# Kernel tuning notes

Measured on AMD Instinct MI355X. Metric: run time of the kernel, lower is better.

Reference implementation:

```python
import jax, jax.numpy as jnp
import numpy as np

B, T, V, E, H, O = 32, 512, 32000, 512, 1024, 128


def setup_inputs() -> dict:
    key = jax.random.key(0)
    ks = jax.random.split(key, 8)
    s = lambda k, shape: (jax.random.normal(k, shape) * 0.02).astype(jnp.float32)
    return {
        "tokens": jax.random.randint(ks[0], (B, T), 0, V),
        "verb_indices": jax.random.randint(ks[1], (B,), 0, T),
        "emb": s(ks[2], (V, E)),
        "W_ih": s(ks[3], (4 * H, E)),
        "W_hh": s(ks[4], (4 * H, H)),
        "b_ih": jnp.zeros((4 * H,), jnp.float32),
        "b_hh": jnp.zeros((4 * H,), jnp.float32),
        "W_lin": s(ks[5], (O, 2 * H)),
        "b_lin": jnp.zeros((O,), jnp.float32),
    }


def _lstm(e, W_ih, W_hh, b_ih, b_hh):
    # e: [B,T,E] -> hidden states [B,T,H]; PyTorch gate order i,f,g,o
    Hd = W_hh.shape[1]
    # precompute input projections for all timesteps (one big GEMM)
    x_proj = jnp.einsum("bte,ge->btg", e, W_ih) + b_ih + b_hh  # [B,T,4H]

    def step(carry, x_t):
        h, c = carry
        gates = x_t + h @ W_hh.T  # [B,4H]
        i, f, g, o = jnp.split(gates, 4, axis=-1)
        i = jax.nn.sigmoid(i)
        f = jax.nn.sigmoid(f)
        g = jnp.tanh(g)
        o = jax.nn.sigmoid(o)
        c = f * c + i * g
        h = o * jnp.tanh(c)
        return (h, c), h

    h0 = jnp.zeros((e.shape[0], Hd), e.dtype)
    (_, _), hs = jax.lax.scan(step, (h0, h0), jnp.swapaxes(x_proj, 0, 1))
    return jnp.swapaxes(hs, 0, 1)  # [B,T,H]


def reference(tokens, verb_indices, emb, W_ih, W_hh, b_ih, b_hh, W_lin, b_lin):
    e = emb[tokens]  # [B,T,E]
    out = _lstm(e, W_ih, W_hh, b_ih, b_hh)  # [B,T,H]
    verbs = out[jnp.arange(out.shape[0]), verb_indices]  # [B,H] verb hidden state
    # linear over concat([verb, out_t]) == split the weight and sum two GEMMs
    Wv, Wo = jnp.split(W_lin, 2, axis=1)  # [O,H] each
    logits = (
        jnp.einsum("bh,oh->bo", verbs, Wv)[:, None, :]
        + jnp.einsum("bth,oh->bto", out, Wo)
        + b_lin
    )  # [B,T,O]
    return jax.nn.log_softmax(logits, axis=-1)
```

## Files before the change

### kernel.cpp

```cpp
#include <hip/hip_runtime.h>


typedef short s8v __attribute__((ext_vector_type(8)));
typedef float f4v __attribute__((ext_vector_type(4)));
typedef unsigned int u4v __attribute__((ext_vector_type(4)));

#define WS_CNT_OFF   131072
#define WS_VROWS_OFF 139264
#define WS_VLOG_OFF  204800

__device__ __forceinline__ float b2f(unsigned short u) {
    union { unsigned int i; float f; } x; x.i = ((unsigned int)u) << 16; return x.f;
}
__device__ __forceinline__ unsigned short f2b(float f) {
    union { float f; unsigned int i; } x; x.f = f;
    unsigned int r = (x.i + 0x7fffu + ((x.i >> 16) & 1u)) >> 16;
    return (unsigned short)r;
}
__device__ __forceinline__ float blo(unsigned int u) {
    union { unsigned int i; float f; } x; x.i = u << 16; return x.f;
}
__device__ __forceinline__ float bhi(unsigned int u) {
    union { unsigned int i; float f; } x; x.i = u & 0xffff0000u; return x.f;
}

__global__ void init_kernel(unsigned int* ws) {
    int i = blockIdx.x * 256 + threadIdx.x;
    if (i < 34816) ws[i] = 0u;
}

__device__ __forceinline__ void project_cols(
    const short* hA, const float* __restrict__ Wr0, const float* __restrict__ Wr1,
    float* __restrict__ dout, int b0, int tproj, int w, int tid)
{
    const int pair = tid >> 4, p = tid & 15;
    const int b = pair >> 1, oc = pair & 1;
    const float* wr = oc ? Wr1 : Wr0;
    float acc = 0.f;
#pragma unroll
    for (int j = 0; j < 8; ++j) {
        int ko = j * 16 + p;
        u4v d = *(const u4v*)&hA[(ko * 17 + b) * 8];
        const float* wk = wr + ko * 8;
        f4v w0 = *(const f4v*)wk, w1 = *(const f4v*)(wk + 4);
        unsigned int d0 = d[0], d1 = d[1], d2 = d[2], d3 = d[3];
        acc += blo(d0) * w0[0] + bhi(d0) * w0[1] + blo(d1) * w0[2] + bhi(d1) * w0[3]
             + blo(d2) * w1[0] + bhi(d2) * w1[1] + blo(d3) * w1[2] + bhi(d3) * w1[3];
    }
#pragma unroll
    for (int off = 1; off < 16; off <<= 1) acc += __shfl_xor(acc, off);
    if (p == 0)
        dout[((size_t)(b0 + b) * 512 + tproj) * 128 + 2 * w + oc] = acc;
}

__global__ __launch_bounds__(256, 1) void scan_kernel(
    const int* __restrict__ tokens,
    const int* __restrict__ vidx,
    const float* __restrict__ emb,
    const float* __restrict__ W_ih,
    const float* __restrict__ W_hh,
    const float* __restrict__ b_ih,
    const float* __restrict__ b_hh,
    const float* __restrict__ W_lin,
    unsigned short* __restrict__ hbuf,
    unsigned int* __restrict__ flags_all,
    unsigned short* __restrict__ vrows,
    float* __restrict__ dout)
{
    __shared__ short hA[128 * 17 * 8];
    __shared__ short eA[2][64 * 17 * 8];
    __shared__ int   tokL[512 * 8];

    const int tid  = threadIdx.x;
    const int g    = blockIdx.x >> 6;
    const int w    = blockIdx.x & 63;
    const int b0   = g * 8;
    const int lane = tid & 63;
    const int v    = tid >> 6;
    const int q    = lane >> 4;
    const int c    = lane & 15;

    const float* Wr0 = W_lin + (size_t)(2 * w) * 2048 + 1024;
    const float* Wr1 = W_lin + (size_t)(2 * w + 1) * 2048 + 1024;

    const int n = ((c >> 2) * 1024) + 16 * w + 4 * v + (c & 3);
    s8v Bh[32], Be[16];
    {
        const float* rh = W_hh + (size_t)n * 1024;
#pragma unroll
        for (int ks = 0; ks < 32; ++ks) {
            const float* s = rh + ks * 32 + q * 8;
            f4v lo = *(const f4v*)s, hi = *(const f4v*)(s + 4);
            s8v f;
#pragma unroll
            for (int j = 0; j < 4; ++j) { f[j] = (short)f2b(lo[j]); f[j + 4] = (short)f2b(hi[j]); }
            Bh[ks] = f;
        }
        const float* re = W_ih + (size_t)n * 512;
#pragma unroll
        for (int ks = 0; ks < 16; ++ks) {
            const float* s = re + ks * 32 + q * 8;
            f4v lo = *(const f4v*)s, hi = *(const f4v*)(s + 4);
            s8v f;
#pragma unroll
            for (int j = 0; j < 4; ++j) { f[j] = (short)f2b(lo[j]); f[j + 4] = (short)f2b(hi[j]); }
            Be[ks] = f;
        }
    }

    for (int i = tid; i < 4096; i += 256)
        tokL[(i & 511) * 8 + (i >> 9)] = tokens[(b0 + (i >> 9)) * 512 + (i & 511)];

    const s8v zv = {0,0,0,0,0,0,0,0};
    for (int i = tid; i < 1024; i += 256) { int ko = i >> 3, r = 8 + (i & 7);
        *(s8v*)&hA[(ko * 17 + r) * 8] = zv; }
    for (int i = tid; i < 512; i += 256) { int ko = i >> 3, r = 8 + (i & 7);
        *(s8v*)&eA[0][(ko * 17 + r) * 8] = zv;
        *(s8v*)&eA[1][(ko * 17 + r) * 8] = zv; }
    __syncthreads();

    for (int i = tid; i < 512; i += 256) {
        int ko = i >> 3, b = i & 7;
        int tok = tokL[b];
        const float* s = emb + (size_t)tok * 512 + ko * 8;
        f4v lo = *(const f4v*)s, hi = *(const f4v*)(s + 4);
        s8v f;
#pragma unroll
        for (int j = 0; j < 4; ++j) { f[j] = (short)f2b(lo[j]); f[j + 4] = (short)f2b(hi[j]); }
        *(s8v*)&eA[0][(ko * 17 + b) * 8] = f;
    }

    const int jloc = 16 * w + 4 * v + (lane & 3);
    const float bI = b_ih[jloc]        + b_hh[jloc];
    const float bF = b_ih[1024 + jloc] + b_hh[1024 + jloc];
    const float bG = b_ih[2048 + jloc] + b_hh[2048 + jloc];
    const float bO = b_ih[3072 + jloc] + b_hh[3072 + jloc];
    const int  shbase = (lane & 48) | (lane & 3);
    const bool stAct  = ((lane & 12) == 0) && (lane < 32) && !(lane & 1);
    const int  phid   = 8 * w + 2 * v + ((lane >> 1) & 1);
    const int  Db     = (phid >> 2) * 32 + (phid & 3) + (lane >> 4) * 16;
    int tv0 = -1, tv1 = -1, tv2 = -1, tv3 = -1;
    if (stAct) {
        int bb = b0 + 4 * (lane >> 4);
        tv0 = vidx[bb]; tv1 = vidx[bb + 1]; tv2 = vidx[bb + 2]; tv3 = vidx[bb + 3];
    }
    const int vrb = (b0 + 4 * (lane >> 4)) * 1024 + jloc;

    float cst[4] = {0.f, 0.f, 0.f, 0.f};
    unsigned short* hb     = hbuf + g * 2 * 8192;
    unsigned int*   hb32   = (unsigned int*)hb;
    unsigned int*   gflags = flags_all + g * 256;
    int rp = 0;
    __syncthreads();

    for (int t = 0; t < 512; ++t) {
        f4v ae = {0.f, 0.f, 0.f, 0.f};
        const short* eAc = eA[t & 1];
#pragma unroll
        for (int ks = 0; ks < 16; ++ks) {
            s8v a = *(const s8v*)&eAc[((ks * 4 + q) * 17 + c) * 8];
            ae = __builtin_amdgcn_mfma_f32_16x16x32_bf16(a, Be[ks], ae, 0, 0, 0);
        }

        if (t > 0) {
            const unsigned tt = (unsigned)t;
            for (;;) {
                unsigned f0 = __hip_atomic_load(&gflags[lane],       __ATOMIC_RELAXED, __HIP_MEMORY_SCOPE_AGENT);
                unsigned f1 = __hip_atomic_load(&gflags[64 + lane],  __ATOMIC_RELAXED, __HIP_MEMORY_SCOPE_AGENT);
                unsigned f2 = __hip_atomic_load(&gflags[128 + lane], __ATOMIC_RELAXED, __HIP_MEMORY_SCOPE_AGENT);
                unsigned f3 = __hip_atomic_load(&gflags[192 + lane], __ATOMIC_RELAXED, __HIP_MEMORY_SCOPE_AGENT);
                unsigned m01 = f0 < f1 ? f0 : f1;
                unsigned m23 = f2 < f3 ? f2 : f3;
                unsigned m = m01 < m23 ? m01 : m23;
                if (__all(m >= tt)) break;
            }
            asm volatile("" ::: "memory");
        }

        {
            const unsigned long long* src =
                (const unsigned long long*)(hb + rp * 8192);
#pragma unroll
            for (int it = 0; it < 8; ++it) {
                int j = it * 256 + tid;
                unsigned long long d = __hip_atomic_load(src + j, __ATOMIC_RELAXED,
                                                         __HIP_MEMORY_SCOPE_AGENT);
                int ko = j >> 4, b = (j >> 1) & 7, posq = (j & 1) << 2;
                *(unsigned long long*)&hA[(ko * 17 + b) * 8 + posq] = d;
            }
        }
        __syncthreads();

        f4v ah0 = {0.f, 0.f, 0.f, 0.f}, ah1 = {0.f, 0.f, 0.f, 0.f};
#pragma unroll
        for (int ks = 0; ks < 16; ++ks) {
            s8v a0 = *(const s8v*)&hA[((2 * ks) * 4 + q) * 17 * 8 + c * 8];
            s8v a1 = *(const s8v*)&hA[((2 * ks + 1) * 4 + q) * 17 * 8 + c * 8];
            ah0 = __builtin_amdgcn_mfma_f32_16x16x32_bf16(a0, Bh[2 * ks], ah0, 0, 0, 0);
            ah1 = __builtin_amdgcn_mfma_f32_16x16x32_bf16(a1, Bh[2 * ks + 1], ah1, 0, 0, 0);
        }

        int hui[4];
#pragma unroll
        for (int r = 0; r < 4; ++r) {
            float s = ae[r] + ah0[r] + ah1[r];
            float xi = __shfl(s, shbase);
            float xf = __shfl(s, shbase + 4);
            float xg = __shfl(s, shbase + 8);
            float xo = __shfl(s, shbase + 12);
            float ig = 1.f / (1.f + __expf(-(xi + bI)));
            float fg = 1.f / (1.f + __expf(-(xf + bF)));
            float gg = 1.f - 2.f / (1.f + __expf(2.f * (xg + bG)));
            float og = 1.f / (1.f + __expf(-(xo + bO)));
            cst[r] = fg * cst[r] + ig * gg;
            float h = og * (1.f - 2.f / (1.f + __expf(2.f * cst[r])));
            hui[r] = (int)f2b(h);
        }
#pragma unroll
        for (int r = 0; r < 4; ++r) {
            int ph = __shfl_xor(hui[r], 1);
            if (stAct) {
                unsigned pack = (unsigned)hui[r] | (((unsigned)ph) << 16);
                __hip_atomic_store(&hb32[(rp ^ 1) * 4096 + Db + r * 4], pack,
                                   __ATOMIC_RELAXED, __HIP_MEMORY_SCOPE_AGENT);
                int tvr = (r == 0) ? tv0 : (r == 1) ? tv1 : (r == 2) ? tv2 : tv3;
                if (t == tvr)
                    *(unsigned int*)&vrows[vrb + r * 1024] = pack;
            }
        }
        asm volatile("s_waitcnt vmcnt(0)" ::: "memory");
        if (lane == 0)
            __hip_atomic_store(&gflags[w * 4 + v], (unsigned)(t + 1),
                               __ATOMIC_RELAXED, __HIP_MEMORY_SCOPE_AGENT);

        if (t >= 1)
            project_cols(hA, Wr0, Wr1, dout, b0, t - 1, w, tid);

        if (t < 511) {
            int tn = t + 1;
            short* eAn = eA[tn & 1];
            for (int i = tid; i < 512; i += 256) {
                int ko = i >> 3, b = i & 7;
                int tok = tokL[tn * 8 + b];
                const float* s2 = emb + (size_t)tok * 512 + ko * 8;
                f4v lo = *(const f4v*)s2, hi = *(const f4v*)(s2 + 4);
                s8v f;
#pragma unroll
                for (int j2 = 0; j2 < 4; ++j2) { f[j2] = (short)f2b(lo[j2]); f[j2 + 4] = (short)f2b(hi[j2]); }
                *(s8v*)&eAn[(ko * 17 + b) * 8] = f;
            }
        }
        __syncthreads();
        rp ^= 1;
    }

    for (;;) {
        unsigned f0 = __hip_atomic_load(&gflags[lane],       __ATOMIC_RELAXED, __HIP_MEMORY_SCOPE_AGENT);
        unsigned f1 = __hip_atomic_load(&gflags[64 + lane],  __ATOMIC_RELAXED, __HIP_MEMORY_SCOPE_AGENT);
        unsigned f2 = __hip_atomic_load(&gflags[128 + lane], __ATOMIC_RELAXED, __HIP_MEMORY_SCOPE_AGENT);
        unsigned f3 = __hip_atomic_load(&gflags[192 + lane], __ATOMIC_RELAXED, __HIP_MEMORY_SCOPE_AGENT);
        unsigned m01 = f0 < f1 ? f0 : f1;
        unsigned m23 = f2 < f3 ? f2 : f3;
        unsigned m = m01 < m23 ? m01 : m23;
        if (__all(m >= 512u)) break;
    }
    asm volatile("" ::: "memory");
    {
        const unsigned long long* src = (const unsigned long long*)(hb + rp * 8192);
#pragma unroll
        for (int it = 0; it < 8; ++it) {
            int j = it * 256 + tid;
            unsigned long long d = __hip_atomic_load(src + j, __ATOMIC_RELAXED,
                                                     __HIP_MEMORY_SCOPE_AGENT);
            int ko = j >> 4, b = (j >> 1) & 7, posq = (j & 1) << 2;
            *(unsigned long long*)&hA[(ko * 17 + b) * 8 + posq] = d;
        }
    }
    __syncthreads();
    project_cols(hA, Wr0, Wr1, dout, b0, 511, w, tid);
}

__global__ void verb_kernel(const unsigned short* __restrict__ vrows,
                            const float* __restrict__ W_lin,
                            const float* __restrict__ b_lin,
                            float* __restrict__ vlog)
{
    __shared__ float vrow[1024];
    int b = blockIdx.x, tid = threadIdx.x;
    for (int i = tid; i < 1024; i += 256) vrow[i] = b2f(vrows[b * 1024 + i]);
    __syncthreads();
    if (tid < 128) {
        float acc = 0.f;
        const float* wr = W_lin + (size_t)tid * 2048;
        for (int h = 0; h < 1024; ++h) acc += vrow[h] * wr[h];
        vlog[b * 128 + tid] = acc + b_lin[tid];
    }
}

__global__ void softmax_kernel(float* __restrict__ dout,
                               const float* __restrict__ vlog)
{
    int tid = threadIdx.x;
    int grow = blockIdx.x * 32 + (tid >> 3);
    int part = tid & 7;
    int b = grow >> 9;
    float* pp = dout + (size_t)grow * 128 + part * 16;
    const float* vb = vlog + b * 128 + part * 16;
    float L[16];
#pragma unroll
    for (int i = 0; i < 16; ++i) L[i] = pp[i] + vb[i];
    float m = L[0];
#pragma unroll
    for (int i = 1; i < 16; ++i) m = fmaxf(m, L[i]);
    for (int off = 1; off < 8; off <<= 1) m = fmaxf(m, __shfl_xor(m, off));
    float s = 0.f;
#pragma unroll
    for (int i = 0; i < 16; ++i) s += expf(L[i] - m);
    for (int off = 1; off < 8; off <<= 1) s += __shfl_xor(s, off);
    float lz = m + logf(s);
#pragma unroll
    for (int i = 0; i < 16; ++i) pp[i] = L[i] - lz;
}

extern "C" void kernel_launch(void* const* d_in, const int* in_sizes, int n_in,
                              void* d_out, int out_size, void* d_ws, size_t ws_size,
                              hipStream_t stream) {
    const int*   tokens = (const int*)d_in[0];
    const int*   vidx   = (const int*)d_in[1];
    const float* emb    = (const float*)d_in[2];
    const float* W_ih   = (const float*)d_in[3];
    const float* W_hh   = (const float*)d_in[4];
    const float* b_ih   = (const float*)d_in[5];
    const float* b_hh   = (const float*)d_in[6];
    const float* W_lin  = (const float*)d_in[7];
    const float* b_lin  = (const float*)d_in[8];
    float* dout = (float*)d_out;

    char* ws = (char*)d_ws;
    unsigned short* hbuf  = (unsigned short*)ws;
    unsigned int*   flags = (unsigned int*)(ws + WS_CNT_OFF);
    unsigned short* vrows = (unsigned short*)(ws + WS_VROWS_OFF);
    float*          vlog  = (float*)(ws + WS_VLOG_OFF);

    init_kernel<<<136, 256, 0, stream>>>((unsigned int*)ws);
    scan_kernel<<<256, 256, 0, stream>>>(tokens, vidx, emb, W_ih, W_hh, b_ih, b_hh,
                                         W_lin, hbuf, flags, vrows, dout);
    verb_kernel<<<32, 256, 0, stream>>>(vrows, W_lin, b_lin, vlog);
    softmax_kernel<<<512, 256, 0, stream>>>(dout, vlog);
}
```

Baseline: 3.800 ms.

## Restructure cross-block LSTM step sync: padded flags, wider stores, overlapped h loads

```diff
diff --git a/kernel.cpp b/kernel.cpp
--- a/kernel.cpp
+++ b/kernel.cpp
@@ -136,57 +136,80 @@
     const float bG = b_ih[2048 + jloc] + b_hh[2048 + jloc];
     const float bO = b_ih[3072 + jloc] + b_hh[3072 + jloc];
     const int  shbase = (lane & 48) | (lane & 3);
-    const bool stAct  = ((lane & 12) == 0) && (lane < 32) && !(lane & 1);
-    const int  phid   = 8 * w + 2 * v + ((lane >> 1) & 1);
-    const int  Db     = (phid >> 2) * 32 + (phid & 3) + (lane >> 4) * 16;
+    const bool stActV = ((lane & 13) == 0) && (lane < 32);
+    const bool stActQ = ((lane & 15) == 0) && (lane < 32);
+    const int  Dq = ((2 * w + (v >> 1)) * 32 + 2 * (v & 1) + 16 * q) >> 1;
     int tv0 = -1, tv1 = -1, tv2 = -1, tv3 = -1;
-    if (stAct) {
+    if (stActV) {
         int bb = b0 + 4 * (lane >> 4);
         tv0 = vidx[bb]; tv1 = vidx[bb + 1]; tv2 = vidx[bb + 2]; tv3 = vidx[bb + 3];
     }
     const int vrb = (b0 + 4 * (lane >> 4)) * 1024 + jloc;
 
     float cst[4] = {0.f, 0.f, 0.f, 0.f};
-    unsigned short* hb     = hbuf + g * 2 * 8192;
-    unsigned int*   hb32   = (unsigned int*)hb;
-    unsigned int*   gflags = flags_all + g * 256;
+    unsigned short*     hb     = hbuf + g * 2 * 8192;
+    unsigned long long* hb64   = (unsigned long long*)hb;
+    unsigned int*       gflags = flags_all + g * 2048;
+    const int fidx = (lane * 4 + v) * 8;
+    const int myflag = (w * 4 + v) * 8;
     int rp = 0;
     __syncthreads();
 
     for (int t = 0; t < 512; ++t) {
-        f4v ae = {0.f, 0.f, 0.f, 0.f};
-        const short* eAc = eA[t & 1];
-#pragma unroll
-        for (int ks = 0; ks < 16; ++ks) {
-            s8v a = *(const s8v*)&eAc[((ks * 4 + q) * 17 + c) * 8];
-            ae = __builtin_amdgcn_mfma_f32_16x16x32_bf16(a, Be[ks], ae, 0, 0, 0);
-        }
-
         if (t > 0) {
             const unsigned tt = (unsigned)t;
-            for (;;) {
-                unsigned f0 = __hip_atomic_load(&gflags[lane],       __ATOMIC_RELAXED, __HIP_MEMORY_SCOPE_AGENT);
-                unsigned f1 = __hip_atomic_load(&gflags[64 + lane],  __ATOMIC_RELAXED, __HIP_MEMORY_SCOPE_AGENT);
-                unsigned f2 = __hip_atomic_load(&gflags[128 + lane], __ATOMIC_RELAXED, __HIP_MEMORY_SCOPE_AGENT);
-                unsigned f3 = __hip_atomic_load(&gflags[192 + lane], __ATOMIC_RELAXED, __HIP_MEMORY_SCOPE_AGENT);
-                unsigned m01 = f0 < f1 ? f0 : f1;
-                unsigned m23 = f2 < f3 ? f2 : f3;
-                unsigned m = m01 < m23 ? m01 : m23;
-                if (__all(m >= tt)) break;
+            for (int spin = 0; ; ++spin) {
+                unsigned f = __hip_atomic_load(&gflags[fidx], __ATOMIC_RELAXED,
+                                               __HIP_MEMORY_SCOPE_AGENT);
+                if (__all(f >= tt)) break;
+                if (spin >= 2) __builtin_amdgcn_s_sleep(2);
             }
             asm volatile("" ::: "memory");
         }
 
+        const unsigned long long* src =
+            (const unsigned long long*)(hb + rp * 8192);
+        const short* eAc = eA[t & 1];
+        f4v ae = {0.f, 0.f, 0.f, 0.f};
         {
-            const unsigned long long* src =
-                (const unsigned long long*)(hb + rp * 8192);
-#pragma unroll
-            for (int it = 0; it < 8; ++it) {
-                int j = it * 256 + tid;
-                unsigned long long d = __hip_atomic_load(src + j, __ATOMIC_RELAXED,
-                                                         __HIP_MEMORY_SCOPE_AGENT);
+            unsigned long long dbuf[4]; int jarr[4];
+#pragma unroll
+            for (int it = 0; it < 4; ++it) {
+                int i = ((it + w) & 7) * 64 + lane;
+                int j = (((((i >> 3) << 1) | (v >> 1)) << 4) | ((i & 7) << 1) | (v & 1));
+                jarr[it] = j;
+                dbuf[it] = __hip_atomic_load(src + j, __ATOMIC_RELAXED,
+                                             __HIP_MEMORY_SCOPE_AGENT);
+            }
+#pragma unroll
+            for (int ks = 0; ks < 8; ++ks) {
+                s8v a = *(const s8v*)&eAc[((ks * 4 + q) * 17 + c) * 8];
+                ae = __builtin_amdgcn_mfma_f32_16x16x32_bf16(a, Be[ks], ae, 0, 0, 0);
+            }
+#pragma unroll
+            for (int it = 0; it < 4; ++it) {
+                int j = jarr[it];
                 int ko = j >> 4, b = (j >> 1) & 7, posq = (j & 1) << 2;
-                *(unsigned long long*)&hA[(ko * 17 + b) * 8 + posq] = d;
+                *(unsigned long long*)&hA[(ko * 17 + b) * 8 + posq] = dbuf[it];
+            }
+#pragma unroll
+            for (int it = 4; it < 8; ++it) {
+                int i = ((it + w) & 7) * 64 + lane;
+                int j = (((((i >> 3) << 1) | (v >> 1)) << 4) | ((i & 7) << 1) | (v & 1));
+                jarr[it - 4] = j;
+                dbuf[it - 4] = __hip_atomic_load(src + j, __ATOMIC_RELAXED,
+                                                 __HIP_MEMORY_SCOPE_AGENT);
+            }
+#pragma unroll
+            for (int ks = 8; ks < 16; ++ks) {
+                s8v a = *(const s8v*)&eAc[((ks * 4 + q) * 17 + c) * 8];
+                ae = __builtin_amdgcn_mfma_f32_16x16x32_bf16(a, Be[ks], ae, 0, 0, 0);
+            }
+#pragma unroll
+            for (int it = 0; it < 4; ++it) {
+                int j = jarr[it];
+                int ko = j >> 4, b = (j >> 1) & 7, posq = (j & 1) << 2;
+                *(unsigned long long*)&hA[(ko * 17 + b) * 8 + posq] = dbuf[it];
             }
         }
         __syncthreads();
@@ -219,10 +242,15 @@
 #pragma unroll
         for (int r = 0; r < 4; ++r) {
             int ph = __shfl_xor(hui[r], 1);
-            if (stAct) {
-                unsigned pack = (unsigned)hui[r] | (((unsigned)ph) << 16);
-                __hip_atomic_store(&hb32[(rp ^ 1) * 4096 + Db + r * 4], pack,
+            unsigned pack = (unsigned)hui[r] | (((unsigned)ph) << 16);
+            unsigned hi = (unsigned)__shfl_xor((int)pack, 2);
+            if (stActQ) {
+                unsigned long long pk = (unsigned long long)pack |
+                                        (((unsigned long long)hi) << 32);
+                __hip_atomic_store(&hb64[(rp ^ 1) * 1024 + Dq + r * 2], pk,
                                    __ATOMIC_RELAXED, __HIP_MEMORY_SCOPE_AGENT);
+            }
+            if (stActV) {
                 int tvr = (r == 0) ? tv0 : (r == 1) ? tv1 : (r == 2) ? tv2 : tv3;
                 if (t == tvr)
                     *(unsigned int*)&vrows[vrb + r * 1024] = pack;
@@ -230,7 +258,7 @@
         }
         asm volatile("s_waitcnt vmcnt(0)" ::: "memory");
         if (lane == 0)
-            __hip_atomic_store(&gflags[w * 4 + v], (unsigned)(t + 1),
+            __hip_atomic_store(&gflags[myflag], (unsigned)(t + 1),
                                __ATOMIC_RELAXED, __HIP_MEMORY_SCOPE_AGENT);
 
         if (t >= 1)
@@ -254,22 +282,19 @@
         rp ^= 1;
     }
 
-    for (;;) {
-        unsigned f0 = __hip_atomic_load(&gflags[lane],       __ATOMIC_RELAXED, __HIP_MEMORY_SCOPE_AGENT);
-        unsigned f1 = __hip_atomic_load(&gflags[64 + lane],  __ATOMIC_RELAXED, __HIP_MEMORY_SCOPE_AGENT);
-        unsigned f2 = __hip_atomic_load(&gflags[128 + lane], __ATOMIC_RELAXED, __HIP_MEMORY_SCOPE_AGENT);
-        unsigned f3 = __hip_atomic_load(&gflags[192 + lane], __ATOMIC_RELAXED, __HIP_MEMORY_SCOPE_AGENT);
-        unsigned m01 = f0 < f1 ? f0 : f1;
-        unsigned m23 = f2 < f3 ? f2 : f3;
-        unsigned m = m01 < m23 ? m01 : m23;
-        if (__all(m >= 512u)) break;
+    for (int spin = 0; ; ++spin) {
+        unsigned f = __hip_atomic_load(&gflags[fidx], __ATOMIC_RELAXED,
+                                       __HIP_MEMORY_SCOPE_AGENT);
+        if (__all(f >= 512u)) break;
+        if (spin >= 2) __builtin_amdgcn_s_sleep(2);
     }
     asm volatile("" ::: "memory");
     {
         const unsigned long long* src = (const unsigned long long*)(hb + rp * 8192);
 #pragma unroll
         for (int it = 0; it < 8; ++it) {
-            int j = it * 256 + tid;
+            int i = ((it + w) & 7) * 64 + lane;
+            int j = (((((i >> 3) << 1) | (v >> 1)) << 4) | ((i & 7) << 1) | (v & 1));
             unsigned long long d = __hip_atomic_load(src + j, __ATOMIC_RELAXED,
                                                      __HIP_MEMORY_SCOPE_AGENT);
             int ko = j >> 4, b = (j >> 1) & 7, posq = (j & 1) << 2;
```

Measured after the change: 3.321 ms. 12.6% less time.
